# Performance work log

Measured on AMD Instinct MI355X. Metric: run time of the kernel, lower is better.

Reference implementation:

```python
import jax, jax.numpy as jnp
import numpy as np

K = 6
D_IN = 128
D_OUT = 128
N_COARSE = 4000
N_FINE = 40000


def setup_inputs() -> dict:
    key = jax.random.key(0)
    k1, k2, k3, k4, k5 = jax.random.split(key, 5)
    x_coarse = jax.random.normal(k1, (N_COARSE, D_IN), dtype=jnp.float32)
    pos_coarse = jax.random.uniform(k2, (N_COARSE, 3), dtype=jnp.float32)
    pos_fine = jax.random.uniform(k3, (N_FINE, 3), dtype=jnp.float32)
    # nnx.Linear params: lecun_normal kernel, zero bias (use small random for generality)
    W = jax.random.normal(k4, (D_IN, D_OUT), dtype=jnp.float32) / np.sqrt(D_IN)
    b = jax.random.normal(k5, (D_OUT,), dtype=jnp.float32) * 0.01
    return {"x_coarse": x_coarse, "pos_coarse": pos_coarse, "pos_fine": pos_fine, "W": W, "b": b}


def reference(x_coarse, pos_coarse, pos_fine, W, b):
    # dense pairwise L2 distances [Nf, Nc] (faithful to the original's full matrix)
    distances = jnp.linalg.norm(pos_fine[:, None, :] - pos_coarse[None, :, :], axis=-1)
    # full argsort then slice, matching the original (incl. tie-break order)
    knn_idx = jnp.argsort(distances, axis=1)[:, :K]        # [Nf, K]
    gathered = x_coarse[knn_idx]                            # [Nf, K, d_in]
    interp = jnp.mean(gathered, axis=1)                     # [Nf, d_in]
    return interp @ W + b                                   # [Nf, d_out]
```

## Files before the change

### kernel.cpp

```cpp
#include <hip/hip_runtime.h>
#include <cstdint>

#define NCOARSE 4000
#define NFINE   40000
#define DIM     128
#define GRES    8
#define CELLH   0.125f
#define CAP_C   40
#define CAP_F   160
#define PPB     16
#define CHUNKS  10
#define SCAP    640
#define NS      172
#define NYG     125

__device__ __forceinline__ uint64_t min64(uint64_t a, uint64_t b) { return a < b ? a : b; }
__device__ __forceinline__ uint64_t max64(uint64_t a, uint64_t b) { return a > b ? a : b; }
__device__ __forceinline__ int cell_coord(float x) {
    int c = (int)(x * 8.0f);
    return c < 0 ? 0 : (c > 7 ? 7 : c);
}

__global__ __launch_bounds__(256) void k_zero(int* __restrict__ p) {
    p[blockIdx.x * 256 + threadIdx.x] = 0;
}

__global__ __launch_bounds__(256) void k_build(const float* __restrict__ pc,
                                               const float* __restrict__ pf,
                                               const float* __restrict__ xc,
                                               const float* __restrict__ W,
                                               int* __restrict__ cntC, int* __restrict__ cntF,
                                               float4* __restrict__ ptsC, float4* __restrict__ srtF,
                                               float* __restrict__ Y) {
    __shared__ float xs[32][DIM];
    const int bid = blockIdx.x, tid = threadIdx.x;
    if (bid < NS) {
        const int i = bid * 256 + tid;
        if (i < NCOARSE) {
            const float x = pc[3*i], y = pc[3*i+1], z = pc[3*i+2];
            const int c = (cell_coord(z) << 6) | (cell_coord(y) << 3) | cell_coord(x);
            const int slot = atomicAdd(&cntC[c], 1);
            if (slot < CAP_C) ptsC[c * CAP_C + slot] = make_float4(x, y, z, __int_as_float(i));
        } else if (i < NCOARSE + NFINE) {
            const int j = i - NCOARSE;
            const float x = pf[3*j], y = pf[3*j+1], z = pf[3*j+2];
            const int c = (cell_coord(z) << 6) | (cell_coord(y) << 3) | cell_coord(x);
            const int slot = atomicAdd(&cntF[c], 1);
            if (slot < CAP_F) srtF[c * CAP_F + slot] = make_float4(x, y, z, __int_as_float(j));
        }
    } else {
        const int g  = bid - NS;
        const int r0 = g * 32;
        #pragma unroll
        for (int t = 0; t < 4; ++t)
            reinterpret_cast<float4*>(xs)[tid + t * 256] =
                reinterpret_cast<const float4*>(xc + r0 * DIM)[tid + t * 256];
        __syncthreads();
        const int rq = tid >> 5;
        const int jq = tid & 31;
        float acc[4][4];
        #pragma unroll
        for (int i = 0; i < 4; ++i)
            #pragma unroll
            for (int j = 0; j < 4; ++j) acc[i][j] = 0.f;
        #pragma unroll 2
        for (int k = 0; k < DIM; ++k) {
            const float4 wv = *reinterpret_cast<const float4*>(W + k * DIM + jq * 4);
            #pragma unroll
            for (int i = 0; i < 4; ++i) {
                const float a = xs[rq + 8 * i][k];
                acc[i][0] += a * wv.x; acc[i][1] += a * wv.y;
                acc[i][2] += a * wv.z; acc[i][3] += a * wv.w;
            }
        }
        #pragma unroll
        for (int i = 0; i < 4; ++i)
            *reinterpret_cast<float4*>(Y + (r0 + rq + 8 * i) * DIM + jq * 4) =
                make_float4(acc[i][0], acc[i][1], acc[i][2], acc[i][3]);
    }
}

__device__ __forceinline__ void popmin_merge(const uint64_t own[7], uint64_t mg[7]) {
    uint64_t a0 = own[0], a1 = own[1], a2 = own[2], a3 = own[3],
             a4 = own[4], a5 = own[5], a6 = own[6];
    #pragma unroll
    for (int r = 0; r < 7; ++r) {
        uint64_t m = a0;
        m = min64(m, __shfl_xor((unsigned long long)m, 1));
        m = min64(m, __shfl_xor((unsigned long long)m, 2));
        m = min64(m, __shfl_xor((unsigned long long)m, 4));
        mg[r] = m;
        const bool win = (a0 == m);
        a0 = win ? a1 : a0;
        a1 = win ? a2 : a1;
        a2 = win ? a3 : a2;
        a3 = win ? a4 : a3;
        a4 = win ? a5 : a4;
        a5 = win ? a6 : a5;
        a6 = win ? ~0ull : a6;
    }
}

__device__ __forceinline__ bool done_check(uint64_t k7, float fx, float fy, float fz,
                                           int ix, int iy, int iz, int s) {
    const float d7 = __uint_as_float((uint32_t)(k7 >> 32));
    float clear = 1e30f;
    if (ix - s >= 0) clear = fminf(clear, __fsub_rn(fx, (float)(ix - s) * CELLH));
    if (ix + s <= 6) clear = fminf(clear, __fsub_rn((float)(ix + s + 1) * CELLH, fx));
    if (iy - s >= 0) clear = fminf(clear, __fsub_rn(fy, (float)(iy - s) * CELLH));
    if (iy + s <= 6) clear = fminf(clear, __fsub_rn((float)(iy + s + 1) * CELLH, fy));
    if (iz - s >= 0) clear = fminf(clear, __fsub_rn(fz, (float)(iz - s) * CELLH));
    if (iz + s <= 6) clear = fminf(clear, __fsub_rn((float)(iz + s + 1) * CELLH, fz));
    return d7 < clear * clear * 0.9999f;
}

#define INS(p) { \
    const float ddx = __fsub_rn(fx, (p).x); \
    const float ddy = __fsub_rn(fy, (p).y); \
    const float ddz = __fsub_rn(fz, (p).z); \
    const float d2  = __fadd_rn(__fadd_rn(__fmul_rn(ddx, ddx), __fmul_rn(ddy, ddy)), \
                                __fmul_rn(ddz, ddz)); \
    const uint64_t v = ((uint64_t)__float_as_uint(d2) << 32) | (uint32_t)__float_as_uint((p).w); \
    if (v < own[6]) { \
        own[6] = min64(own[6], max64(own[5], v)); \
        own[5] = min64(own[5], max64(own[4], v)); \
        own[4] = min64(own[4], max64(own[3], v)); \
        own[3] = min64(own[3], max64(own[2], v)); \
        own[2] = min64(own[2], max64(own[1], v)); \
        own[1] = min64(own[1], max64(own[0], v)); \
        own[0] = min64(own[0], v); \
    } }

__global__ __launch_bounds__(128) void k_main(
    const float*  __restrict__ Y,
    const float*  __restrict__ bias,
    const int*    __restrict__ cntC,
    const int*    __restrict__ cntF,
    const float4* __restrict__ ptsG,
    const float4* __restrict__ srtF,
    float* __restrict__ out)
{
    __shared__ float4 spts[SCAP];
    __shared__ int rBeg[32], rLds[32];
    __shared__ int idx6[PPB][6];
    __shared__ int forig[PPB];
    __shared__ int metaT[1];

    const int bid  = blockIdx.x;
    const int tid  = threadIdx.x;
    const int cell = bid & 511;
    const int chunk= bid >> 9;

    const int ctot = min(cntF[cell], CAP_F);
    const int base = chunk * PPB;
    const int npts = min(PPB, ctot - base);
    if (npts <= 0) return;

    const int fl  = tid >> 3;
    const int par = tid & 7;
    const int ix = cell & 7, iy = (cell >> 3) & 7, iz = cell >> 6;

    const int srcf = min(fl, npts - 1);
    const float4 fp = srtF[cell * CAP_F + base + srcf];
    const float fx = fp.x, fy = fp.y, fz = fp.z;
    if (par == 0) forig[fl] = (fl < npts) ? __float_as_int(fp.w) : -1;

    const int bx0 = max(ix - 1, 0), bx1 = min(ix + 1, 7);
    const int by0 = max(iy - 1, 0), by1 = min(iy + 1, 7);
    const int bz0 = max(iz - 1, 0), bz1 = min(iz + 1, 7);
    const int nx = bx1 - bx0 + 1, ny = by1 - by0 + 1, nz = bz1 - bz0 + 1;
    const int ncell = nx * ny * nz;

    if (tid < 32) {
        const bool valid = tid < ncell;
        int len = 0, bg = 0;
        if (valid) {
            const int ex = bx0 + tid % nx;
            const int rem = tid / nx;
            const int ey = by0 + rem % ny;
            const int ez = bz0 + rem / ny;
            const int cc = (ez << 6) | (ey << 3) | ex;
            len = min(cntC[cc], CAP_C);
            bg  = cc * CAP_C;
        }
        int x = len;
        #pragma unroll
        for (int o = 1; o < 32; o <<= 1) {
            const int v = __shfl_up(x, o);
            if (tid >= o) x += v;
        }
        rBeg[tid] = valid ? bg : 0;
        rLds[tid] = valid ? (x - len) : 0x7fffffff;
        if (tid == ncell - 1) metaT[0] = x;
    }
    __syncthreads();

    const int total  = metaT[0];
    const bool staged = (total <= SCAP);
    if (staged) {
        for (int g = tid; g < total; g += 128) {
            int lo = 0, hi = 31;
            while (lo < hi) { const int mid = (lo + hi + 1) >> 1; if (rLds[mid] <= g) lo = mid; else hi = mid - 1; }
            spts[g] = ptsG[rBeg[lo] + (g - rLds[lo])];
        }
    }
    __syncthreads();

    uint64_t own[7];
    #pragma unroll
    for (int r = 0; r < 7; ++r) own[r] = ~0ull;

    if (staged) {
        #pragma unroll 4
        for (int i = par; i < total; i += 8) { float4 p = spts[i]; INS(p) }
    } else {
        for (int cz = bz0; cz <= bz1; ++cz)
            for (int cy = by0; cy <= by1; ++cy)
                for (int cx = bx0; cx <= bx1; ++cx) {
                    const int cc = (cz << 6) | (cy << 3) | cx;
                    const int len = min(cntC[cc], CAP_C);
                    const int bg  = cc * CAP_C;
                    for (int i = par; i < len; i += 8) { float4 p = ptsG[bg + i]; INS(p) }
                }
    }

    uint64_t mg[7];
    popmin_merge(own, mg);
    bool done = done_check(mg[6], fx, fy, fz, ix, iy, iz, 1);

    for (int s = 2; s <= 7; ++s) {
        if (__all(done)) break;
        if (!done) {
            for (int dz = -s; dz <= s; ++dz) {
                const int cz = iz + dz;
                if ((unsigned)cz >= (unsigned)GRES) continue;
                const bool fz_face = (dz == -s) | (dz == s);
                for (int dy = -s; dy <= s; ++dy) {
                    const int cy = iy + dy;
                    if ((unsigned)cy >= (unsigned)GRES) continue;
                    const bool yz_face = fz_face | (dy == -s) | (dy == s);
                    for (int dx = -s; dx <= s; ++dx) {
                        if (!yz_face && dx > -s && dx < s) continue;
                        const int cx = ix + dx;
                        if ((unsigned)cx >= (unsigned)GRES) continue;
                        if (cx >= bx0 && cx <= bx1 && cy >= by0 && cy <= by1 &&
                            cz >= bz0 && cz <= bz1) continue;
                        const int cc = (cz << 6) | (cy << 3) | cx;
                        const int len = min(cntC[cc], CAP_C);
                        const int bg  = cc * CAP_C;
                        for (int i = par; i < len; i += 8) { float4 p = ptsG[bg + i]; INS(p) }
                    }
                }
            }
            popmin_merge(own, mg);
            done = done_check(mg[6], fx, fy, fz, ix, iy, iz, s);
        }
    }

    if (par == 0) {
        int i5 = (int)(uint32_t)mg[5];
        const int i6 = (int)(uint32_t)mg[6];
        const float d5 = sqrtf(__uint_as_float((uint32_t)(mg[5] >> 32)));
        const float d6 = sqrtf(__uint_as_float((uint32_t)(mg[6] >> 32)));
        if (d5 == d6 && i6 < i5) i5 = i6;
        idx6[fl][0] = (int)(uint32_t)mg[0];
        idx6[fl][1] = (int)(uint32_t)mg[1];
        idx6[fl][2] = (int)(uint32_t)mg[2];
        idx6[fl][3] = (int)(uint32_t)mg[3];
        idx6[fl][4] = (int)(uint32_t)mg[4];
        idx6[fl][5] = i5;
    }
    __syncthreads();

    {
        const int fr = forig[fl];
        if (fr >= 0) {
            const int id0 = idx6[fl][0], id1 = idx6[fl][1], id2 = idx6[fl][2];
            const int id3 = idx6[fl][3], id4 = idx6[fl][4], id5 = idx6[fl][5];
            constexpr float inv6 = 1.0f / 6.0f;
            #pragma unroll
            for (int k = 0; k < 4; ++k) {
                const int q = (k * 8 + par) * 4;
                const float4 y0 = *reinterpret_cast<const float4*>(Y + id0 * DIM + q);
                const float4 y1 = *reinterpret_cast<const float4*>(Y + id1 * DIM + q);
                const float4 y2 = *reinterpret_cast<const float4*>(Y + id2 * DIM + q);
                const float4 y3 = *reinterpret_cast<const float4*>(Y + id3 * DIM + q);
                const float4 y4 = *reinterpret_cast<const float4*>(Y + id4 * DIM + q);
                const float4 y5 = *reinterpret_cast<const float4*>(Y + id5 * DIM + q);
                const float4 bv = *reinterpret_cast<const float4*>(bias + q);
                float4 o;
                o.x = (y0.x + y1.x + y2.x + y3.x + y4.x + y5.x) * inv6 + bv.x;
                o.y = (y0.y + y1.y + y2.y + y3.y + y4.y + y5.y) * inv6 + bv.y;
                o.z = (y0.z + y1.z + y2.z + y3.z + y4.z + y5.z) * inv6 + bv.z;
                o.w = (y0.w + y1.w + y2.w + y3.w + y4.w + y5.w) * inv6 + bv.w;
                *reinterpret_cast<float4*>(out + fr * DIM + q) = o;
            }
        }
    }
}

extern "C" void kernel_launch(void* const* d_in, const int* in_sizes, int n_in,
                              void* d_out, int out_size, void* d_ws, size_t ws_size,
                              hipStream_t stream) {
    const float* xc = (const float*)d_in[0];
    const float* pc = (const float*)d_in[1];
    const float* pf = (const float*)d_in[2];
    const float* W  = (const float*)d_in[3];
    const float* b  = (const float*)d_in[4];
    float* out = (float*)d_out;

    int*    cntC = (int*)d_ws;
    int*    cntF = (int*)((char*)d_ws + 2048);
    float4* ptsC = (float4*)((char*)d_ws + 4096);
    float4* srtF = (float4*)((char*)d_ws + 331776);
    float*  Y    = (float*)((char*)d_ws + 1642496);

    k_zero <<<dim3(4),            dim3(256), 0, stream>>>((int*)d_ws);
    k_build<<<dim3(NS + NYG),     dim3(256), 0, stream>>>(pc, pf, xc, W, cntC, cntF, ptsC, srtF, Y);
    k_main <<<dim3(512 * CHUNKS), dim3(128), 0, stream>>>(Y, b, cntC, cntF, ptsC, srtF, out);
}
```

Measured before the change: 59.78 us.

## Replace atomic grid binning with ballot-based deterministic slots and drop fine-point sorting

Coarse points are now binned without atomics: each block loads all coarse cell ids into shared memory and computes each point's slot and each cell's count with wave ballots. This removes the zeroing kernel. Fine points are no longer sorted into cells; k_main processes 32 fine points per 256-thread block in input order and reads coarse neighbours straight from global memory, dropping the shared-memory staging. The goal is fewer launches and no atomics, at the cost of redundant per-block scans of all 4000 coarse cell ids and less spatial coherence between fine points that share a block.

```diff
diff --git a/kernel.cpp b/kernel.cpp
--- a/kernel.cpp
+++ b/kernel.cpp
@@ -7,12 +7,10 @@
 #define GRES    8
 #define CELLH   0.125f
 #define CAP_C   40
-#define CAP_F   160
-#define PPB     16
-#define CHUNKS  10
-#define SCAP    640
-#define NS      172
-#define NYG     125
+#define NB_A    500
+#define NB_B    128
+#define NB_Y    125
+#define NBUILD  (NB_A + NB_B + NB_Y)
 
 __device__ __forceinline__ uint64_t min64(uint64_t a, uint64_t b) { return a < b ? a : b; }
 __device__ __forceinline__ uint64_t max64(uint64_t a, uint64_t b) { return a > b ? a : b; }
@@ -21,39 +19,66 @@
     return c < 0 ? 0 : (c > 7 ? 7 : c);
 }
 
-__global__ __launch_bounds__(256) void k_zero(int* __restrict__ p) {
-    p[blockIdx.x * 256 + threadIdx.x] = 0;
-}
+union BuildSM {
+    uint16_t cellS[4096];
+    float    xs[32][DIM];
+};
 
 __global__ __launch_bounds__(256) void k_build(const float* __restrict__ pc,
-                                               const float* __restrict__ pf,
                                                const float* __restrict__ xc,
                                                const float* __restrict__ W,
-                                               int* __restrict__ cntC, int* __restrict__ cntF,
-                                               float4* __restrict__ ptsC, float4* __restrict__ srtF,
-                                               float* __restrict__ Y) {
-    __shared__ float xs[32][DIM];
+                                               int*    __restrict__ cntC,
+                                               float4* __restrict__ ptsC,
+                                               float*  __restrict__ Y) {
+    __shared__ BuildSM sm;
     const int bid = blockIdx.x, tid = threadIdx.x;
-    if (bid < NS) {
-        const int i = bid * 256 + tid;
-        if (i < NCOARSE) {
-            const float x = pc[3*i], y = pc[3*i+1], z = pc[3*i+2];
-            const int c = (cell_coord(z) << 6) | (cell_coord(y) << 3) | cell_coord(x);
-            const int slot = atomicAdd(&cntC[c], 1);
-            if (slot < CAP_C) ptsC[c * CAP_C + slot] = make_float4(x, y, z, __int_as_float(i));
-        } else if (i < NCOARSE + NFINE) {
-            const int j = i - NCOARSE;
-            const float x = pf[3*j], y = pf[3*j+1], z = pf[3*j+2];
-            const int c = (cell_coord(z) << 6) | (cell_coord(y) << 3) | cell_coord(x);
-            const int slot = atomicAdd(&cntF[c], 1);
-            if (slot < CAP_F) srtF[c * CAP_F + slot] = make_float4(x, y, z, __int_as_float(j));
+
+    if (bid < NB_A + NB_B) {
+        #pragma unroll
+        for (int t = 0; t < 16; ++t) {
+            const int idx = t * 256 + tid;
+            uint16_t cv = 0xFFFF;
+            if (idx < NCOARSE) {
+                cv = (uint16_t)((cell_coord(pc[3*idx+2]) << 6) |
+                                (cell_coord(pc[3*idx+1]) << 3) |
+                                 cell_coord(pc[3*idx]));
+            }
+            sm.cellS[idx] = cv;
+        }
+        __syncthreads();
+        const int wid = tid >> 6, lane = tid & 63;
+
+        if (bid < NB_A) {
+            const int i0 = bid * 8 + wid * 2;
+            #pragma unroll
+            for (int pp = 0; pp < 2; ++pp) {
+                const int i  = i0 + pp;
+                const uint16_t ci = sm.cellS[i];
+                int slot = 0;
+                for (int it = 0; it < 63; ++it) {
+                    const int j = it * 64 + lane;
+                    const bool lt = (j < i) && (sm.cellS[j] == ci);
+                    slot += (int)__popcll(__ballot(lt));
+                }
+                if (lane == 0 && slot < CAP_C)
+                    ptsC[(int)ci * CAP_C + slot] =
+                        make_float4(pc[3*i], pc[3*i+1], pc[3*i+2], __int_as_float(i));
+            }
+        } else {
+            const int c = (bid - NB_A) * 4 + wid;
+            int len = 0;
+            for (int it = 0; it < 63; ++it) {
+                const int j = it * 64 + lane;
+                len += (int)__popcll(__ballot(sm.cellS[j] == (uint16_t)c));
+            }
+            if (lane == 0) cntC[c] = len;
         }
     } else {
-        const int g  = bid - NS;
+        const int g  = bid - (NB_A + NB_B);
         const int r0 = g * 32;
         #pragma unroll
         for (int t = 0; t < 4; ++t)
-            reinterpret_cast<float4*>(xs)[tid + t * 256] =
+            reinterpret_cast<float4*>(sm.xs)[tid + t * 256] =
                 reinterpret_cast<const float4*>(xc + r0 * DIM)[tid + t * 256];
         __syncthreads();
         const int rq = tid >> 5;
@@ -68,7 +93,7 @@
             const float4 wv = *reinterpret_cast<const float4*>(W + k * DIM + jq * 4);
             #pragma unroll
             for (int i = 0; i < 4; ++i) {
-                const float a = xs[rq + 8 * i][k];
+                const float a = sm.xs[rq + 8 * i][k];
                 acc[i][0] += a * wv.x; acc[i][1] += a * wv.y;
                 acc[i][2] += a * wv.z; acc[i][3] += a * wv.w;
             }
@@ -131,98 +156,38 @@
         own[0] = min64(own[0], v); \
     } }
 
-__global__ __launch_bounds__(128) void k_main(
+__global__ __launch_bounds__(256) void k_main(
     const float*  __restrict__ Y,
     const float*  __restrict__ bias,
     const int*    __restrict__ cntC,
-    const int*    __restrict__ cntF,
     const float4* __restrict__ ptsG,
-    const float4* __restrict__ srtF,
+    const float*  __restrict__ pf,
     float* __restrict__ out)
 {
-    __shared__ float4 spts[SCAP];
-    __shared__ int rBeg[32], rLds[32];
-    __shared__ int idx6[PPB][6];
-    __shared__ int forig[PPB];
-    __shared__ int metaT[1];
-
-    const int bid  = blockIdx.x;
-    const int tid  = threadIdx.x;
-    const int cell = bid & 511;
-    const int chunk= bid >> 9;
-
-    const int ctot = min(cntF[cell], CAP_F);
-    const int base = chunk * PPB;
-    const int npts = min(PPB, ctot - base);
-    if (npts <= 0) return;
-
+    const int tid = threadIdx.x;
     const int fl  = tid >> 3;
     const int par = tid & 7;
-    const int ix = cell & 7, iy = (cell >> 3) & 7, iz = cell >> 6;
-
-    const int srcf = min(fl, npts - 1);
-    const float4 fp = srtF[cell * CAP_F + base + srcf];
-    const float fx = fp.x, fy = fp.y, fz = fp.z;
-    if (par == 0) forig[fl] = (fl < npts) ? __float_as_int(fp.w) : -1;
+    const int f   = blockIdx.x * 32 + fl;
+
+    const float fx = pf[3*f], fy = pf[3*f+1], fz = pf[3*f+2];
+    const int ix = cell_coord(fx), iy = cell_coord(fy), iz = cell_coord(fz);
 
     const int bx0 = max(ix - 1, 0), bx1 = min(ix + 1, 7);
     const int by0 = max(iy - 1, 0), by1 = min(iy + 1, 7);
     const int bz0 = max(iz - 1, 0), bz1 = min(iz + 1, 7);
-    const int nx = bx1 - bx0 + 1, ny = by1 - by0 + 1, nz = bz1 - bz0 + 1;
-    const int ncell = nx * ny * nz;
-
-    if (tid < 32) {
-        const bool valid = tid < ncell;
-        int len = 0, bg = 0;
-        if (valid) {
-            const int ex = bx0 + tid % nx;
-            const int rem = tid / nx;
-            const int ey = by0 + rem % ny;
-            const int ez = bz0 + rem / ny;
-            const int cc = (ez << 6) | (ey << 3) | ex;
-            len = min(cntC[cc], CAP_C);
-            bg  = cc * CAP_C;
-        }
-        int x = len;
-        #pragma unroll
-        for (int o = 1; o < 32; o <<= 1) {
-            const int v = __shfl_up(x, o);
-            if (tid >= o) x += v;
-        }
-        rBeg[tid] = valid ? bg : 0;
-        rLds[tid] = valid ? (x - len) : 0x7fffffff;
-        if (tid == ncell - 1) metaT[0] = x;
-    }
-    __syncthreads();
-
-    const int total  = metaT[0];
-    const bool staged = (total <= SCAP);
-    if (staged) {
-        for (int g = tid; g < total; g += 128) {
-            int lo = 0, hi = 31;
-            while (lo < hi) { const int mid = (lo + hi + 1) >> 1; if (rLds[mid] <= g) lo = mid; else hi = mid - 1; }
-            spts[g] = ptsG[rBeg[lo] + (g - rLds[lo])];
-        }
-    }
-    __syncthreads();
 
     uint64_t own[7];
     #pragma unroll
     for (int r = 0; r < 7; ++r) own[r] = ~0ull;
 
-    if (staged) {
-        #pragma unroll 4
-        for (int i = par; i < total; i += 8) { float4 p = spts[i]; INS(p) }
-    } else {
-        for (int cz = bz0; cz <= bz1; ++cz)
-            for (int cy = by0; cy <= by1; ++cy)
-                for (int cx = bx0; cx <= bx1; ++cx) {
-                    const int cc = (cz << 6) | (cy << 3) | cx;
-                    const int len = min(cntC[cc], CAP_C);
-                    const int bg  = cc * CAP_C;
-                    for (int i = par; i < len; i += 8) { float4 p = ptsG[bg + i]; INS(p) }
-                }
-    }
+    for (int cz = bz0; cz <= bz1; ++cz)
+        for (int cy = by0; cy <= by1; ++cy)
+            for (int cx = bx0; cx <= bx1; ++cx) {
+                const int cc = (cz << 6) | (cy << 3) | cx;
+                const int len = min(cntC[cc], CAP_C);
+                const int bg  = cc * CAP_C;
+                for (int i = par; i < len; i += 8) { float4 p = ptsG[bg + i]; INS(p) }
+            }
 
     uint64_t mg[7];
     popmin_merge(own, mg);
@@ -257,45 +222,37 @@
         }
     }
 
-    if (par == 0) {
-        int i5 = (int)(uint32_t)mg[5];
+    int i5 = (int)(uint32_t)mg[5];
+    {
         const int i6 = (int)(uint32_t)mg[6];
         const float d5 = sqrtf(__uint_as_float((uint32_t)(mg[5] >> 32)));
         const float d6 = sqrtf(__uint_as_float((uint32_t)(mg[6] >> 32)));
         if (d5 == d6 && i6 < i5) i5 = i6;
-        idx6[fl][0] = (int)(uint32_t)mg[0];
-        idx6[fl][1] = (int)(uint32_t)mg[1];
-        idx6[fl][2] = (int)(uint32_t)mg[2];
-        idx6[fl][3] = (int)(uint32_t)mg[3];
-        idx6[fl][4] = (int)(uint32_t)mg[4];
-        idx6[fl][5] = i5;
-    }
-    __syncthreads();
-
-    {
-        const int fr = forig[fl];
-        if (fr >= 0) {
-            const int id0 = idx6[fl][0], id1 = idx6[fl][1], id2 = idx6[fl][2];
-            const int id3 = idx6[fl][3], id4 = idx6[fl][4], id5 = idx6[fl][5];
-            constexpr float inv6 = 1.0f / 6.0f;
-            #pragma unroll
-            for (int k = 0; k < 4; ++k) {
-                const int q = (k * 8 + par) * 4;
-                const float4 y0 = *reinterpret_cast<const float4*>(Y + id0 * DIM + q);
-                const float4 y1 = *reinterpret_cast<const float4*>(Y + id1 * DIM + q);
-                const float4 y2 = *reinterpret_cast<const float4*>(Y + id2 * DIM + q);
-                const float4 y3 = *reinterpret_cast<const float4*>(Y + id3 * DIM + q);
-                const float4 y4 = *reinterpret_cast<const float4*>(Y + id4 * DIM + q);
-                const float4 y5 = *reinterpret_cast<const float4*>(Y + id5 * DIM + q);
-                const float4 bv = *reinterpret_cast<const float4*>(bias + q);
-                float4 o;
-                o.x = (y0.x + y1.x + y2.x + y3.x + y4.x + y5.x) * inv6 + bv.x;
-                o.y = (y0.y + y1.y + y2.y + y3.y + y4.y + y5.y) * inv6 + bv.y;
-                o.z = (y0.z + y1.z + y2.z + y3.z + y4.z + y5.z) * inv6 + bv.z;
-                o.w = (y0.w + y1.w + y2.w + y3.w + y4.w + y5.w) * inv6 + bv.w;
-                *reinterpret_cast<float4*>(out + fr * DIM + q) = o;
-            }
-        }
+    }
+    const int id0 = (int)(uint32_t)mg[0];
+    const int id1 = (int)(uint32_t)mg[1];
+    const int id2 = (int)(uint32_t)mg[2];
+    const int id3 = (int)(uint32_t)mg[3];
+    const int id4 = (int)(uint32_t)mg[4];
+    const int id5 = i5;
+
+    constexpr float inv6 = 1.0f / 6.0f;
+    #pragma unroll
+    for (int k = 0; k < 4; ++k) {
+        const int q = (k * 8 + par) * 4;
+        const float4 y0 = *reinterpret_cast<const float4*>(Y + id0 * DIM + q);
+        const float4 y1 = *reinterpret_cast<const float4*>(Y + id1 * DIM + q);
+        const float4 y2 = *reinterpret_cast<const float4*>(Y + id2 * DIM + q);
+        const float4 y3 = *reinterpret_cast<const float4*>(Y + id3 * DIM + q);
+        const float4 y4 = *reinterpret_cast<const float4*>(Y + id4 * DIM + q);
+        const float4 y5 = *reinterpret_cast<const float4*>(Y + id5 * DIM + q);
+        const float4 bv = *reinterpret_cast<const float4*>(bias + q);
+        float4 o;
+        o.x = (y0.x + y1.x + y2.x + y3.x + y4.x + y5.x) * inv6 + bv.x;
+        o.y = (y0.y + y1.y + y2.y + y3.y + y4.y + y5.y) * inv6 + bv.y;
+        o.z = (y0.z + y1.z + y2.z + y3.z + y4.z + y5.z) * inv6 + bv.z;
+        o.w = (y0.w + y1.w + y2.w + y3.w + y4.w + y5.w) * inv6 + bv.w;
+        *reinterpret_cast<float4*>(out + f * DIM + q) = o;
     }
 }
 
@@ -310,12 +267,9 @@
     float* out = (float*)d_out;
 
     int*    cntC = (int*)d_ws;
-    int*    cntF = (int*)((char*)d_ws + 2048);
     float4* ptsC = (float4*)((char*)d_ws + 4096);
-    float4* srtF = (float4*)((char*)d_ws + 331776);
-    float*  Y    = (float*)((char*)d_ws + 1642496);
-
-    k_zero <<<dim3(4),            dim3(256), 0, stream>>>((int*)d_ws);
-    k_build<<<dim3(NS + NYG),     dim3(256), 0, stream>>>(pc, pf, xc, W, cntC, cntF, ptsC, srtF, Y);
-    k_main <<<dim3(512 * CHUNKS), dim3(128), 0, stream>>>(Y, b, cntC, cntF, ptsC, srtF, out);
-}
+    float*  Y    = (float*)((char*)d_ws + 331776);
+
+    k_build<<<dim3(NBUILD), dim3(256), 0, stream>>>(pc, xc, W, cntC, ptsC, Y);
+    k_main <<<dim3(NFINE / 32), dim3(256), 0, stream>>>(Y, b, cntC, ptsC, pf, out);
+}
```

Measured after the change: 64.85 us. 8.5% more time.
